# Optimization experiments

Measured on AMD Instinct MI355X. Metric: run time of the kernel, lower is better.

The kernel has to match this reference:

```python
import jax, jax.numpy as jnp
import numpy as np

N_NODES = 50000
N_EDGES = 400000
C_IN = 256
HID = 512
C_OUT = 128
N_GRAPHS = 64
BN_EPS = 1e-5


def setup_inputs() -> dict:
    key = jax.random.key(0)
    ks = jax.random.split(key, 18)
    s_in = 1.0 / np.sqrt(C_IN)
    s_h = 1.0 / np.sqrt(HID)
    inp = {
        'x': jax.random.normal(ks[0], (N_NODES, C_IN), jnp.float32),
        'edge_index': jax.random.randint(ks[1], (2, N_EDGES), 0, N_NODES, jnp.int32).astype(jnp.int64),
        'batch': jnp.sort(jax.random.randint(ks[2], (N_NODES,), 0, N_GRAPHS, jnp.int32)).astype(jnp.int64),
        'enc_w': jax.random.normal(ks[3], (C_IN, HID), jnp.float32) * s_in,
        'enc_b': jax.random.normal(ks[4], (HID,), jnp.float32) * s_in,
        'conv_w0': jax.random.normal(ks[5], (2, HID, HID), jnp.float32) * s_h,
        'conv_b0': jax.random.normal(ks[6], (2, HID), jnp.float32) * s_h,
        'bn0_g': jax.random.uniform(ks[7], (2, HID), jnp.float32, 0.5, 1.5),
        'bn0_b': jax.random.normal(ks[8], (2, HID), jnp.float32) * 0.1,
        'conv_w1': jax.random.normal(ks[9], (2, HID, HID), jnp.float32) * s_h,
        'conv_b1': jax.random.normal(ks[10], (2, HID), jnp.float32) * s_h,
        'bn1_g': jax.random.uniform(ks[11], (2, HID), jnp.float32, 0.5, 1.5),
        'bn1_b': jax.random.normal(ks[12], (2, HID), jnp.float32) * 0.1,
        'lin_w': jax.random.normal(ks[13], (HID, HID), jnp.float32) * s_h,
        'lin_b': jax.random.normal(ks[14], (HID,), jnp.float32) * s_h,
        'clf_w': jax.random.normal(ks[15], (HID, C_OUT), jnp.float32) * s_h,
        'clf_b': jax.random.normal(ks[16], (C_OUT,), jnp.float32) * s_h,
    }
    return inp


def _bn_eval(h, gamma, beta):
    # BatchNorm1d in eval mode with default buffers: running_mean=0, running_var=1
    return h * (gamma / jnp.sqrt(1.0 + BN_EPS)) + beta


def reference(x, edge_index, batch, enc_w, enc_b, conv_w0, conv_b0, bn0_g, bn0_b,
              conv_w1, conv_b1, bn1_g, bn1_b, lin_w, lin_b, clf_w, clf_b):
    src, dst = edge_index[0], edge_index[1]
    n = x.shape[0]
    # encoder (gbn output is dead code in the original forward; omitted)
    x = x @ enc_w + enc_b  # [N, HID]
    # GIN_Net: 2 GINConv layers, eps=0, sum aggregation, MLP = Lin-BN-ReLU-Lin-BN
    for i in range(2):
        agg = jax.ops.segment_sum(x[src], dst, num_segments=n)  # scatter-add of neighbor feats
        h = x + agg  # (1 + eps) * x + aggr, eps = 0
        h = h @ conv_w0[i] + conv_b0[i]
        h = jax.nn.relu(_bn_eval(h, bn0_g[i], bn0_b[i]))
        h = h @ conv_w1[i] + conv_b1[i]
        h = _bn_eval(h, bn1_g[i], bn1_b[i])
        # inter-layer relu (dropout p=0 / eval -> identity); skipped after last layer
        x = h if i == 1 else jax.nn.relu(h)
    # global mean pooling over graphs
    sums = jax.ops.segment_sum(x, batch, num_segments=N_GRAPHS)  # [G, HID]
    counts = jax.ops.segment_sum(jnp.ones((n,), x.dtype), batch, num_segments=N_GRAPHS)
    pooled = sums / jnp.maximum(counts, 1.0)[:, None]
    g = jax.nn.gelu(pooled @ lin_w + lin_b, approximate=False)
    # dropout(0.5) identity in eval mode
    return g @ clf_w + clf_b  # [G, C_OUT]
```

## Files before the change

### kernel.cpp

```cpp
#include <hip/hip_runtime.h>
#include <hip/hip_bf16.h>
#include <stdint.h>

#define NN 50000
#define M_PAD 50176
#define NE 400000
#define CIN 256
#define KF 320
#define HID 512
#define COUT 128
#define NG 64
#define SCAN_NB ((NN + 255) / 256)
#define GEMM_NWG 392

typedef short bf16x8 __attribute__((ext_vector_type(8)));
typedef float f32x4 __attribute__((ext_vector_type(4)));

__device__ inline float bf2f(unsigned short u) {
    union { unsigned int i; float f; } v; v.i = ((unsigned int)u) << 16; return v.f;
}
__device__ inline unsigned short f2bf(float f) {
    union { float f; unsigned int u; } v; v.f = f;
    unsigned int r = v.u + 0x7fffu + ((v.u >> 16) & 1u);
    return (unsigned short)(r >> 16);
}

__device__ inline void async16(const void* g, void* l) {
    __builtin_amdgcn_global_load_lds((const __attribute__((address_space(1))) void*)g,
                                     (__attribute__((address_space(3))) void*)l, 16, 0, 0);
}


__global__ void k_f32_to_bf16(const float* __restrict__ in, unsigned short* __restrict__ out, int n4) {
    int i = blockIdx.x * blockDim.x + threadIdx.x;
    if (i < n4) {
        float4 v = ((const float4*)in)[i];
        ushort4 o;
        o.x = f2bf(v.x); o.y = f2bf(v.y); o.z = f2bf(v.z); o.w = f2bf(v.w);
        ((ushort4*)out)[i] = o;
    }
}

__global__ void k_transpose_cvt(const float* __restrict__ in, unsigned short* __restrict__ out, int K, int N) {
    __shared__ float tile[32][33];
    int bx = blockIdx.x * 32, by = blockIdx.y * 32;
    int tx = threadIdx.x & 31, ty = threadIdx.x >> 5;
    for (int i = 0; i < 32; i += 8)
        tile[ty + i][tx] = in[(size_t)(by + ty + i) * N + bx + tx];
    __syncthreads();
    for (int i = 0; i < 32; i += 8)
        out[(size_t)(bx + ty + i) * K + by + tx] = f2bf(tile[tx][ty + i]);
}

__global__ void k_fuse_w0(const float* __restrict__ enc_w, const float* __restrict__ enc_b,
                          const float* __restrict__ W0, unsigned short* __restrict__ WfT) {
    int n = blockIdx.x;
    __shared__ float col[HID];
    for (int j = threadIdx.x; j < HID; j += 256) col[j] = W0[(size_t)j * HID + n];
    __syncthreads();
    int k = threadIdx.x;
    float acc = 0.f;
    for (int j = 0; j < HID; j++) acc += enc_w[(size_t)k * HID + j] * col[j];
    WfT[(size_t)n * KF + k] = f2bf(acc);
    if (k == 0) {
        float v = 0.f;
        for (int j = 0; j < HID; j++) v += enc_b[j] * col[j];
        WfT[(size_t)n * KF + 256] = f2bf(v);
    }
    if (k >= 1 && k < 64) WfT[(size_t)n * KF + 256 + k] = 0;
}

__global__ void k_affine(const float* __restrict__ enc_b,
                         const float* __restrict__ cb0, const float* __restrict__ bg0, const float* __restrict__ bb0,
                         const float* __restrict__ cb1, const float* __restrict__ bg1, const float* __restrict__ bb1,
                         float* __restrict__ scale, float* __restrict__ shift) {
    int c = threadIdx.x;
    const float inv = 0.9999950000374997f;
    scale[c] = 1.f; shift[c] = enc_b[c];
    for (int l = 0; l < 2; l++) {
        float s0 = bg0[l * HID + c] * inv;
        scale[(1 + 2 * l) * HID + c] = s0;
        shift[(1 + 2 * l) * HID + c] = cb0[l * HID + c] * s0 + bb0[l * HID + c];
        float s1 = bg1[l * HID + c] * inv;
        scale[(2 + 2 * l) * HID + c] = s1;
        shift[(2 + 2 * l) * HID + c] = cb1[l * HID + c] * s1 + bb1[l * HID + c];
    }
}


__global__ void k_hist(const int* __restrict__ dst, int* __restrict__ indeg, int n) {
    int i = blockIdx.x * blockDim.x + threadIdx.x;
    if (i < n) atomicAdd(&indeg[dst[i]], 1);
}

__global__ void k_scan1(const int* __restrict__ indeg, int* __restrict__ local,
                        int* __restrict__ blocksum, int n) {
    __shared__ int s[256];
    int t = threadIdx.x;
    int i = blockIdx.x * 256 + t;
    int v = (i < n) ? indeg[i] : 0;
    s[t] = v;
    __syncthreads();
    for (int d = 1; d < 256; d <<= 1) {
        int u = (t >= d) ? s[t - d] : 0;
        __syncthreads();
        s[t] += u;
        __syncthreads();
    }
    if (i < n) local[i] = s[t] - v;
    if (t == 255) blocksum[blockIdx.x] = s[255];
}

__global__ void k_scan2(int* __restrict__ blocksum, int nb) {
    __shared__ int s[256];
    int t = threadIdx.x;
    int v = (t < nb) ? blocksum[t] : 0;
    s[t] = v;
    __syncthreads();
    for (int d = 1; d < 256; d <<= 1) {
        int u = (t >= d) ? s[t - d] : 0;
        __syncthreads();
        s[t] += u;
        __syncthreads();
    }
    if (t < nb) blocksum[t] = s[t] - v;
}

__global__ void k_scan3(const int* __restrict__ local, const int* __restrict__ blocksum,
                        const int* __restrict__ indeg, int* __restrict__ off,
                        int* __restrict__ cursor, int n) {
    int i = blockIdx.x * 256 + threadIdx.x;
    if (i < n) {
        int o = local[i] + blocksum[blockIdx.x];
        off[i] = o;
        cursor[i] = o;
        if (i == n - 1) off[n] = o + indeg[i];
    }
}

__global__ void k_fill(const int* __restrict__ src, const int* __restrict__ dst,
                       int* __restrict__ cursor, int* __restrict__ csr, int n) {
    int i = blockIdx.x * blockDim.x + threadIdx.x;
    if (i < n) {
        int p = atomicAdd(&cursor[dst[i]], 1);
        csr[p] = src[i];
    }
}


__global__ void k_aggregate0(const unsigned short* __restrict__ x, const int* __restrict__ off,
                             const int* __restrict__ csr, unsigned short* __restrict__ z) {
    int wid = (int)((blockIdx.x * blockDim.x + threadIdx.x) >> 6);
    if (wid >= NN) return;
    int lane = threadIdx.x & 63;
    const uint2* xr = (const uint2*)x;
    uint2 v = xr[(size_t)wid * 64 + lane];
    float acc[4];
    {
        unsigned short* p = (unsigned short*)&v;
        for (int i = 0; i < 4; i++) acc[i] = bf2f(p[i]);
    }
    int e0 = off[wid], e1 = off[wid + 1];
    int e = e0;
    for (; e + 3 < e1; e += 4) {
        int u0 = csr[e], u1 = csr[e + 1], u2 = csr[e + 2], u3 = csr[e + 3];
        uint2 v0 = xr[(size_t)u0 * 64 + lane];
        uint2 v1 = xr[(size_t)u1 * 64 + lane];
        uint2 v2 = xr[(size_t)u2 * 64 + lane];
        uint2 v3 = xr[(size_t)u3 * 64 + lane];
        unsigned short* p0 = (unsigned short*)&v0;
        unsigned short* p1 = (unsigned short*)&v1;
        unsigned short* p2 = (unsigned short*)&v2;
        unsigned short* p3 = (unsigned short*)&v3;
#pragma unroll
        for (int i = 0; i < 4; i++)
            acc[i] += (bf2f(p0[i]) + bf2f(p1[i])) + (bf2f(p2[i]) + bf2f(p3[i]));
    }
    for (; e < e1; e++) {
        int u = csr[e];
        uint2 vu = xr[(size_t)u * 64 + lane];
        unsigned short* p = (unsigned short*)&vu;
#pragma unroll
        for (int i = 0; i < 4; i++) acc[i] += bf2f(p[i]);
    }
    uint2 o;
    unsigned short* po = (unsigned short*)&o;
    for (int i = 0; i < 4; i++) po[i] = f2bf(acc[i]);
    uint2* zr = (uint2*)z;
    zr[(size_t)wid * 80 + lane] = o;
    if (lane < 16) {
        uint2 ex; ex.x = 0; ex.y = 0;
        if (lane == 0) ex.x = (unsigned)f2bf((float)(1 + e1 - e0));
        zr[(size_t)wid * 80 + 64 + lane] = ex;
    }
}


__global__ void k_aggregate(const unsigned short* __restrict__ x, const int* __restrict__ off,
                            const int* __restrict__ csr, unsigned short* __restrict__ h) {
    int wid = (int)((blockIdx.x * blockDim.x + threadIdx.x) >> 6);
    if (wid >= NN) return;
    int lane = threadIdx.x & 63;
    const uint4* xr = (const uint4*)x;
    uint4 v = xr[(size_t)wid * 64 + lane];
    float acc[8];
    {
        unsigned short* p = (unsigned short*)&v;
        for (int i = 0; i < 8; i++) acc[i] = bf2f(p[i]);
    }
    int e0 = off[wid], e1 = off[wid + 1];
    int e = e0;
    for (; e + 3 < e1; e += 4) {
        int u0 = csr[e], u1 = csr[e + 1], u2 = csr[e + 2], u3 = csr[e + 3];
        uint4 v0 = xr[(size_t)u0 * 64 + lane];
        uint4 v1 = xr[(size_t)u1 * 64 + lane];
        uint4 v2 = xr[(size_t)u2 * 64 + lane];
        uint4 v3 = xr[(size_t)u3 * 64 + lane];
        unsigned short* p0 = (unsigned short*)&v0;
        unsigned short* p1 = (unsigned short*)&v1;
        unsigned short* p2 = (unsigned short*)&v2;
        unsigned short* p3 = (unsigned short*)&v3;
#pragma unroll
        for (int i = 0; i < 8; i++)
            acc[i] += (bf2f(p0[i]) + bf2f(p1[i])) + (bf2f(p2[i]) + bf2f(p3[i]));
    }
    for (; e < e1; e++) {
        int u = csr[e];
        uint4 vu = xr[(size_t)u * 64 + lane];
        unsigned short* p = (unsigned short*)&vu;
#pragma unroll
        for (int i = 0; i < 8; i++) acc[i] += bf2f(p[i]);
    }
    uint4 o;
    unsigned short* po = (unsigned short*)&o;
    for (int i = 0; i < 8; i++) po[i] = f2bf(acc[i]);
    ((uint4*)h)[(size_t)wid * 64 + lane] = o;
}


template <int RELU, int NSTEPS>
__global__ __launch_bounds__(512, 2) void k_gemm(const unsigned short* __restrict__ A,
                                                 const unsigned short* __restrict__ WT,
                                                 const float* __restrict__ scale,
                                                 const float* __restrict__ shift,
                                                 unsigned short* __restrict__ out) {
    constexpr int K = NSTEPS * 64;
    __shared__ char lds[131072];
    const int tid = threadIdx.x, w = tid >> 6, lane = tid & 63;
    const int wr = w >> 2, wc = w & 3;
    const int lr = lane & 15, lh = lane >> 4;

    int orig = blockIdx.x;
    int wgid = (orig & 7) * 49 + (orig >> 3);
    int tile_m = (wgid >> 1) * 256;
    int n0 = (wgid & 1) * 256;

    const unsigned short* gA[4];
    const unsigned short* gB[4];
    int ldsoff[4];
#pragma unroll
    for (int ci = 0; ci < 4; ci++) {
        int c = w * 4 + ci;
        int f = c >> 1, kf = c & 1;
        ldsoff[ci] = c * 1024;
        gA[ci] = A + (size_t)(tile_m + f * 16 + lr) * K + kf * 32 + lh * 8;
        gB[ci] = WT + (size_t)(n0 + f * 16 + lr) * K + kf * 32 + lh * 8;
    }

    f32x4 acc[8][4];
#pragma unroll
    for (int x = 0; x < 8; x++)
#pragma unroll
        for (int y = 0; y < 4; y++) acc[x][y] = f32x4{0.f, 0.f, 0.f, 0.f};

#pragma unroll
    for (int ci = 0; ci < 4; ci++) async16(gA[ci], lds + ldsoff[ci]);
#pragma unroll
    for (int ci = 0; ci < 4; ci++) async16(gB[ci], lds + 32768 + ldsoff[ci]);
#pragma unroll
    for (int ci = 0; ci < 4; ci++) async16(gA[ci] + 64, lds + 65536 + ldsoff[ci]);
#pragma unroll
    for (int ci = 0; ci < 4; ci++) async16(gB[ci] + 64, lds + 65536 + 32768 + ldsoff[ci]);

#pragma unroll
    for (int ks = 0; ks < NSTEPS; ks++) {
        const int cur = (ks & 1) << 16;
        if (ks < NSTEPS - 1) asm volatile("s_waitcnt vmcnt(8)" ::: "memory");
        else                 asm volatile("s_waitcnt vmcnt(0)" ::: "memory");
        __builtin_amdgcn_s_barrier();
        __builtin_amdgcn_sched_barrier(0);
#pragma unroll
        for (int kf = 0; kf < 2; kf++) {
            bf16x8 a[8], bb[4];
#pragma unroll
            for (int mf = 0; mf < 8; mf++)
                a[mf] = *(const bf16x8*)(lds + cur + ((wr * 8 + mf) * 2 + kf) * 1024 + lane * 16);
#pragma unroll
            for (int nf = 0; nf < 4; nf++)
                bb[nf] = *(const bf16x8*)(lds + cur + 32768 + ((wc * 4 + nf) * 2 + kf) * 1024 + lane * 16);
#pragma unroll
            for (int mf = 0; mf < 8; mf++)
#pragma unroll
                for (int nf = 0; nf < 4; nf++)
                    acc[mf][nf] = __builtin_amdgcn_mfma_f32_16x16x32_bf16(bb[nf], a[mf], acc[mf][nf], 0, 0, 0);
        }
        __builtin_amdgcn_sched_barrier(0);
        __builtin_amdgcn_s_barrier();
        if (ks + 2 < NSTEPS) {
            int ko = (ks + 2) << 6;
#pragma unroll
            for (int ci = 0; ci < 4; ci++) async16(gA[ci] + ko, lds + cur + ldsoff[ci]);
#pragma unroll
            for (int ci = 0; ci < 4; ci++) async16(gB[ci] + ko, lds + cur + 32768 + ldsoff[ci]);
        }
    }

#pragma unroll
    for (int nf = 0; nf < 4; nf++) {
        int col = n0 + wc * 64 + nf * 16 + lh * 4;
        float4 sc = *(const float4*)&scale[col];
        float4 sh = *(const float4*)&shift[col];
#pragma unroll
        for (int mf = 0; mf < 8; mf++) {
            int row = tile_m + wr * 128 + mf * 16 + lr;
            float y0 = acc[mf][nf][0] * sc.x + sh.x;
            float y1 = acc[mf][nf][1] * sc.y + sh.y;
            float y2 = acc[mf][nf][2] * sc.z + sh.z;
            float y3 = acc[mf][nf][3] * sc.w + sh.w;
            if (RELU) {
                y0 = fmaxf(y0, 0.f); y1 = fmaxf(y1, 0.f);
                y2 = fmaxf(y2, 0.f); y3 = fmaxf(y3, 0.f);
            }
            ushort4 pk;
            pk.x = f2bf(y0); pk.y = f2bf(y1); pk.z = f2bf(y2); pk.w = f2bf(y3);
            *(ushort4*)(out + (size_t)row * HID + col) = pk;
        }
    }
}


__global__ void k_bounds(const int* __restrict__ batch, int* __restrict__ bounds) {
    int t = threadIdx.x;
    if (t <= NG) {
        int lo = 0, hi = NN;
        while (lo < hi) { int mid = (lo + hi) >> 1; if (batch[mid] < t) lo = mid + 1; else hi = mid; }
        bounds[t] = lo;
    }
}

__global__ void k_pool(const unsigned short* __restrict__ x, const int* __restrict__ bounds,
                       float* __restrict__ pooled) {
    int g = blockIdx.x, s = blockIdx.y, t = threadIdx.x;
    int b0 = bounds[g], b1 = bounds[g + 1];
    int len = b1 - b0;
    int r0 = b0 + (int)((long long)len * s / 8);
    int r1 = b0 + (int)((long long)len * (s + 1) / 8);
    float acc = 0.f;
    for (int r = r0; r < r1; r++) acc += bf2f(x[(size_t)r * HID + t]);
    if (r1 > r0) atomicAdd(&pooled[g * HID + t], acc);
}

__global__ void k_tailgemm(const float* __restrict__ pooledSum, const int* __restrict__ bounds,
                           const float* __restrict__ W1, const float* __restrict__ scale,
                           const float* __restrict__ shift, float* __restrict__ xfp) {
    int g = blockIdx.x, t = threadIdx.x;
    __shared__ float row[HID];
    int cnt = bounds[g + 1] - bounds[g];
    float invc = 1.f / fmaxf((float)cnt, 1.f);
    row[t] = pooledSum[g * HID + t] * invc;
    __syncthreads();
    float acc = 0.f;
    for (int k = 0; k < HID; k++) acc += row[k] * W1[(size_t)k * HID + t];
    xfp[g * HID + t] = acc * scale[t] + shift[t];
}

__global__ void k_head1(const float* __restrict__ xfp, const float* __restrict__ lin_w,
                        const float* __restrict__ lin_b, float* __restrict__ gout) {
    int g = blockIdx.x, t = threadIdx.x;
    __shared__ float row[HID];
    row[t] = xfp[g * HID + t];
    __syncthreads();
    float acc = lin_b[t];
    for (int k = 0; k < HID; k++) acc += row[k] * lin_w[(size_t)k * HID + t];
    gout[g * HID + t] = 0.5f * acc * (1.f + erff(acc * 0.7071067811865475f));
}

__global__ void k_head2(const float* __restrict__ gbuf, const float* __restrict__ clf_w,
                        const float* __restrict__ clf_b, float* __restrict__ out) {
    int g = blockIdx.x, t = threadIdx.x;
    __shared__ float row[HID];
    for (int k = t; k < HID; k += 128) row[k] = gbuf[g * HID + k];
    __syncthreads();
    float acc = clf_b[t];
    for (int k = 0; k < HID; k++) acc += row[k] * clf_w[(size_t)k * COUT + t];
    out[g * COUT + t] = acc;
}


extern "C" void kernel_launch(void* const* d_in, const int* in_sizes, int n_in,
                              void* d_out, int out_size, void* d_ws, size_t ws_size,
                              hipStream_t stream) {
    const float* x_f32   = (const float*)d_in[0];
    const int*   ei      = (const int*)d_in[1];
    const int*   batch   = (const int*)d_in[2];
    const float* enc_w   = (const float*)d_in[3];
    const float* enc_b   = (const float*)d_in[4];
    const float* conv_w0 = (const float*)d_in[5];
    const float* conv_b0 = (const float*)d_in[6];
    const float* bn0_g   = (const float*)d_in[7];
    const float* bn0_b   = (const float*)d_in[8];
    const float* conv_w1 = (const float*)d_in[9];
    const float* conv_b1 = (const float*)d_in[10];
    const float* bn1_g   = (const float*)d_in[11];
    const float* bn1_b   = (const float*)d_in[12];
    const float* lin_w   = (const float*)d_in[13];
    const float* lin_b   = (const float*)d_in[14];
    const float* clf_w   = (const float*)d_in[15];
    const float* clf_b   = (const float*)d_in[16];
    const int* srcp = ei;
    const int* dstp = ei + NE;

    char* ws = (char*)d_ws;
    size_t o = 0;
    auto alloc = [&](size_t b) { size_t r = o; o += (b + 255) & ~(size_t)255; return r; };
    unsigned short* buf0 = (unsigned short*)(ws + alloc((size_t)M_PAD * HID * 2));
    unsigned short* buf1 = (unsigned short*)(ws + alloc((size_t)M_PAD * HID * 2));
    unsigned short* buf2 = (unsigned short*)(ws + alloc((size_t)M_PAD * HID * 2));
    unsigned short* xbf  = buf0;
    unsigned short* zbuf = buf2;
    unsigned short* WfT  = (unsigned short*)(ws + alloc((size_t)HID * KF * 2));
    unsigned short* c0T  = (unsigned short*)(ws + alloc((size_t)HID * HID * 2));
    unsigned short* c1T  = (unsigned short*)(ws + alloc((size_t)HID * HID * 2));
    float* aff_scale = (float*)(ws + alloc(5 * HID * 4));
    float* aff_shift = (float*)(ws + alloc(5 * HID * 4));
    int* indeg  = (int*)(ws + alloc((size_t)NN * 4));
    int* off    = (int*)(ws + alloc((size_t)(NN + 1) * 4));
    int* cursor = (int*)(ws + alloc((size_t)NN * 4));
    int* csr    = (int*)(ws + alloc((size_t)NE * 4));
    int* scan_local = (int*)(ws + alloc((size_t)NN * 4));
    int* scan_bsum  = (int*)(ws + alloc((size_t)256 * 4));
    int* bounds = (int*)(ws + alloc((size_t)(NG + 1) * 4));
    float* pooledSum = (float*)(ws + alloc((size_t)NG * HID * 4));
    float* xfp       = (float*)(ws + alloc((size_t)NG * HID * 4));
    float* gbuf      = (float*)(ws + alloc((size_t)NG * HID * 4));
    (void)ws_size; (void)n_in; (void)in_sizes; (void)out_size;

    hipMemsetAsync(indeg, 0, (size_t)NN * 4, stream);
    hipMemsetAsync(pooledSum, 0, (size_t)NG * HID * 4, stream);

    k_f32_to_bf16<<<(NN * CIN / 4 + 255) / 256, 256, 0, stream>>>(x_f32, xbf, NN * CIN / 4);
    k_fuse_w0<<<HID, 256, 0, stream>>>(enc_w, enc_b, conv_w0, WfT);
    k_transpose_cvt<<<dim3(16, 16), 256, 0, stream>>>(conv_w0 + HID * HID, c0T, HID, HID);
    k_transpose_cvt<<<dim3(16, 16), 256, 0, stream>>>(conv_w1, c1T, HID, HID);
    k_affine<<<1, 512, 0, stream>>>(enc_b, conv_b0, bn0_g, bn0_b, conv_b1, bn1_g, bn1_b,
                                    aff_scale, aff_shift);

    k_hist<<<(NE + 255) / 256, 256, 0, stream>>>(dstp, indeg, NE);
    k_scan1<<<SCAN_NB, 256, 0, stream>>>(indeg, scan_local, scan_bsum, NN);
    k_scan2<<<1, 256, 0, stream>>>(scan_bsum, SCAN_NB);
    k_scan3<<<SCAN_NB, 256, 0, stream>>>(scan_local, scan_bsum, indeg, off, cursor, NN);
    k_fill<<<(NE + 255) / 256, 256, 0, stream>>>(srcp, dstp, cursor, csr, NE);
    k_bounds<<<1, 128, 0, stream>>>(batch, bounds);

    k_aggregate0<<<(NN * 64) / 256, 256, 0, stream>>>(xbf, off, csr, zbuf);
    k_gemm<1, KF / 64><<<GEMM_NWG, 512, 0, stream>>>(zbuf, WfT,
                                                     aff_scale + 1 * HID, aff_shift + 1 * HID, buf0);
    k_gemm<1, HID / 64><<<GEMM_NWG, 512, 0, stream>>>(buf0, c1T,
                                                      aff_scale + 2 * HID, aff_shift + 2 * HID, buf2);

    k_aggregate<<<(NN * 64) / 256, 256, 0, stream>>>(buf2, off, csr, buf1);
    k_gemm<1, HID / 64><<<GEMM_NWG, 512, 0, stream>>>(buf1, c0T,
                                                      aff_scale + 3 * HID, aff_shift + 3 * HID, buf2);

    k_pool<<<dim3(NG, 8), 512, 0, stream>>>(buf2, bounds, pooledSum);
    k_tailgemm<<<NG, 512, 0, stream>>>(pooledSum, bounds, conv_w1 + HID * HID,
                                       aff_scale + 4 * HID, aff_shift + 4 * HID, xfp);
    k_head1<<<NG, 512, 0, stream>>>(xfp, lin_w, lin_b, gbuf);
    k_head2<<<NG, 128, 0, stream>>>(gbuf, clf_w, clf_b, (float*)d_out);
}
```

Before: 453.5 us.

## Merge small prep and tail kernels, fold scan pass, deepen gather unroll

Cuts the number of kernel launches. The bf16 conversion and the degree histogram become one grid, the two weight transposes share one launch, the graph-bounds search moves into the affine kernel, and the three tail matvec kernels become one. The separate block-sum scan kernel is removed: each scan3 block now reduces the preceding block sums itself. The neighbour-gather loops in both aggregation kernels unroll to 8 loads so more memory requests are in flight, at the cost of higher register pressure.

```diff
diff --git a/kernel.cpp b/kernel.cpp
--- a/kernel.cpp
+++ b/kernel.cpp
@@ -11,6 +11,8 @@
 #define COUT 128
 #define NG 64
 #define SCAN_NB ((NN + 255) / 256)
+#define CVT_NB (NN * CIN / 4 / 256)
+#define HIST_NB ((NE + 255) / 256)
 #define GEMM_NWG 392
 
 typedef short bf16x8 __attribute__((ext_vector_type(8)));
@@ -31,25 +33,33 @@
 }
 
 
-__global__ void k_f32_to_bf16(const float* __restrict__ in, unsigned short* __restrict__ out, int n4) {
-    int i = blockIdx.x * blockDim.x + threadIdx.x;
-    if (i < n4) {
-        float4 v = ((const float4*)in)[i];
+__global__ void k_prep0(const float* __restrict__ xf, unsigned short* __restrict__ xbf,
+                        const int* __restrict__ dst, int* __restrict__ indeg) {
+    int b = blockIdx.x;
+    if (b < CVT_NB) {
+        int i = b * 256 + threadIdx.x;
+        float4 v = ((const float4*)xf)[i];
         ushort4 o;
         o.x = f2bf(v.x); o.y = f2bf(v.y); o.z = f2bf(v.z); o.w = f2bf(v.w);
-        ((ushort4*)out)[i] = o;
-    }
-}
-
-__global__ void k_transpose_cvt(const float* __restrict__ in, unsigned short* __restrict__ out, int K, int N) {
+        ((ushort4*)xbf)[i] = o;
+    } else {
+        int i = (b - CVT_NB) * 256 + threadIdx.x;
+        if (i < NE) atomicAdd(&indeg[dst[i]], 1);
+    }
+}
+
+__global__ void k_transpose2(const float* __restrict__ s0, const float* __restrict__ s1,
+                             unsigned short* __restrict__ d0, unsigned short* __restrict__ d1) {
+    const float* in = blockIdx.z ? s1 : s0;
+    unsigned short* out = blockIdx.z ? d1 : d0;
     __shared__ float tile[32][33];
     int bx = blockIdx.x * 32, by = blockIdx.y * 32;
     int tx = threadIdx.x & 31, ty = threadIdx.x >> 5;
     for (int i = 0; i < 32; i += 8)
-        tile[ty + i][tx] = in[(size_t)(by + ty + i) * N + bx + tx];
+        tile[ty + i][tx] = in[(size_t)(by + ty + i) * HID + bx + tx];
     __syncthreads();
     for (int i = 0; i < 32; i += 8)
-        out[(size_t)(bx + ty + i) * K + by + tx] = f2bf(tile[tx][ty + i]);
+        out[(size_t)(bx + ty + i) * HID + by + tx] = f2bf(tile[tx][ty + i]);
 }
 
 __global__ void k_fuse_w0(const float* __restrict__ enc_w, const float* __restrict__ enc_b,
@@ -70,10 +80,11 @@
     if (k >= 1 && k < 64) WfT[(size_t)n * KF + 256 + k] = 0;
 }
 
-__global__ void k_affine(const float* __restrict__ enc_b,
-                         const float* __restrict__ cb0, const float* __restrict__ bg0, const float* __restrict__ bb0,
-                         const float* __restrict__ cb1, const float* __restrict__ bg1, const float* __restrict__ bb1,
-                         float* __restrict__ scale, float* __restrict__ shift) {
+__global__ void k_affine_bounds(const float* __restrict__ enc_b,
+                                const float* __restrict__ cb0, const float* __restrict__ bg0, const float* __restrict__ bb0,
+                                const float* __restrict__ cb1, const float* __restrict__ bg1, const float* __restrict__ bb1,
+                                float* __restrict__ scale, float* __restrict__ shift,
+                                const int* __restrict__ batch, int* __restrict__ bounds) {
     int c = threadIdx.x;
     const float inv = 0.9999950000374997f;
     scale[c] = 1.f; shift[c] = enc_b[c];
@@ -85,13 +96,13 @@
         scale[(2 + 2 * l) * HID + c] = s1;
         shift[(2 + 2 * l) * HID + c] = cb1[l * HID + c] * s1 + bb1[l * HID + c];
     }
-}
-
-
-__global__ void k_hist(const int* __restrict__ dst, int* __restrict__ indeg, int n) {
-    int i = blockIdx.x * blockDim.x + threadIdx.x;
-    if (i < n) atomicAdd(&indeg[dst[i]], 1);
-}
+    if (c <= NG) {
+        int lo = 0, hi = NN;
+        while (lo < hi) { int mid = (lo + hi) >> 1; if (batch[mid] < c) lo = mid + 1; else hi = mid; }
+        bounds[c] = lo;
+    }
+}
+
 
 __global__ void k_scan1(const int* __restrict__ indeg, int* __restrict__ local,
                         int* __restrict__ blocksum, int n) {
@@ -111,27 +122,21 @@
     if (t == 255) blocksum[blockIdx.x] = s[255];
 }
 
-__global__ void k_scan2(int* __restrict__ blocksum, int nb) {
-    __shared__ int s[256];
-    int t = threadIdx.x;
-    int v = (t < nb) ? blocksum[t] : 0;
-    s[t] = v;
-    __syncthreads();
-    for (int d = 1; d < 256; d <<= 1) {
-        int u = (t >= d) ? s[t - d] : 0;
-        __syncthreads();
-        s[t] += u;
-        __syncthreads();
-    }
-    if (t < nb) blocksum[t] = s[t] - v;
-}
-
 __global__ void k_scan3(const int* __restrict__ local, const int* __restrict__ blocksum,
                         const int* __restrict__ indeg, int* __restrict__ off,
                         int* __restrict__ cursor, int n) {
-    int i = blockIdx.x * 256 + threadIdx.x;
+    __shared__ int s[256];
+    int t = threadIdx.x;
+    s[t] = (t < blockIdx.x && t < SCAN_NB) ? blocksum[t] : 0;
+    __syncthreads();
+    for (int d = 128; d > 0; d >>= 1) {
+        if (t < d) s[t] += s[t + d];
+        __syncthreads();
+    }
+    int ps = s[0];
+    int i = blockIdx.x * 256 + t;
     if (i < n) {
-        int o = local[i] + blocksum[blockIdx.x];
+        int o = local[i] + ps;
         off[i] = o;
         cursor[i] = o;
         if (i == n - 1) off[n] = o + indeg[i];
@@ -162,19 +167,16 @@
     }
     int e0 = off[wid], e1 = off[wid + 1];
     int e = e0;
-    for (; e + 3 < e1; e += 4) {
-        int u0 = csr[e], u1 = csr[e + 1], u2 = csr[e + 2], u3 = csr[e + 3];
-        uint2 v0 = xr[(size_t)u0 * 64 + lane];
-        uint2 v1 = xr[(size_t)u1 * 64 + lane];
-        uint2 v2 = xr[(size_t)u2 * 64 + lane];
-        uint2 v3 = xr[(size_t)u3 * 64 + lane];
-        unsigned short* p0 = (unsigned short*)&v0;
-        unsigned short* p1 = (unsigned short*)&v1;
-        unsigned short* p2 = (unsigned short*)&v2;
-        unsigned short* p3 = (unsigned short*)&v3;
-#pragma unroll
-        for (int i = 0; i < 4; i++)
-            acc[i] += (bf2f(p0[i]) + bf2f(p1[i])) + (bf2f(p2[i]) + bf2f(p3[i]));
+    for (; e + 7 < e1; e += 8) {
+        uint2 vv[8];
+#pragma unroll
+        for (int q = 0; q < 8; q++) vv[q] = xr[(size_t)csr[e + q] * 64 + lane];
+#pragma unroll
+        for (int q = 0; q < 8; q++) {
+            unsigned short* p = (unsigned short*)&vv[q];
+#pragma unroll
+            for (int i = 0; i < 4; i++) acc[i] += bf2f(p[i]);
+        }
     }
     for (; e < e1; e++) {
         int u = csr[e];
@@ -210,19 +212,16 @@
     }
     int e0 = off[wid], e1 = off[wid + 1];
     int e = e0;
-    for (; e + 3 < e1; e += 4) {
-        int u0 = csr[e], u1 = csr[e + 1], u2 = csr[e + 2], u3 = csr[e + 3];
-        uint4 v0 = xr[(size_t)u0 * 64 + lane];
-        uint4 v1 = xr[(size_t)u1 * 64 + lane];
-        uint4 v2 = xr[(size_t)u2 * 64 + lane];
-        uint4 v3 = xr[(size_t)u3 * 64 + lane];
-        unsigned short* p0 = (unsigned short*)&v0;
-        unsigned short* p1 = (unsigned short*)&v1;
-        unsigned short* p2 = (unsigned short*)&v2;
-        unsigned short* p3 = (unsigned short*)&v3;
-#pragma unroll
-        for (int i = 0; i < 8; i++)
-            acc[i] += (bf2f(p0[i]) + bf2f(p1[i])) + (bf2f(p2[i]) + bf2f(p3[i]));
+    for (; e + 7 < e1; e += 8) {
+        uint4 vv[8];
+#pragma unroll
+        for (int q = 0; q < 8; q++) vv[q] = xr[(size_t)csr[e + q] * 64 + lane];
+#pragma unroll
+        for (int q = 0; q < 8; q++) {
+            unsigned short* p = (unsigned short*)&vv[q];
+#pragma unroll
+            for (int i = 0; i < 8; i++) acc[i] += bf2f(p[i]);
+        }
     }
     for (; e < e1; e++) {
         int u = csr[e];
@@ -339,15 +338,6 @@
 }
 
 
-__global__ void k_bounds(const int* __restrict__ batch, int* __restrict__ bounds) {
-    int t = threadIdx.x;
-    if (t <= NG) {
-        int lo = 0, hi = NN;
-        while (lo < hi) { int mid = (lo + hi) >> 1; if (batch[mid] < t) lo = mid + 1; else hi = mid; }
-        bounds[t] = lo;
-    }
-}
-
 __global__ void k_pool(const unsigned short* __restrict__ x, const int* __restrict__ bounds,
                        float* __restrict__ pooled) {
     int g = blockIdx.x, s = blockIdx.y, t = threadIdx.x;
@@ -360,40 +350,35 @@
     if (r1 > r0) atomicAdd(&pooled[g * HID + t], acc);
 }
 
-__global__ void k_tailgemm(const float* __restrict__ pooledSum, const int* __restrict__ bounds,
-                           const float* __restrict__ W1, const float* __restrict__ scale,
-                           const float* __restrict__ shift, float* __restrict__ xfp) {
+__global__ void k_tail(const float* __restrict__ pooledSum, const int* __restrict__ bounds,
+                       const float* __restrict__ W1, const float* __restrict__ scale,
+                       const float* __restrict__ shift,
+                       const float* __restrict__ lin_w, const float* __restrict__ lin_b,
+                       const float* __restrict__ clf_w, const float* __restrict__ clf_b,
+                       float* __restrict__ out) {
     int g = blockIdx.x, t = threadIdx.x;
-    __shared__ float row[HID];
+    __shared__ float r0[HID], r1[HID], r2[HID];
     int cnt = bounds[g + 1] - bounds[g];
     float invc = 1.f / fmaxf((float)cnt, 1.f);
-    row[t] = pooledSum[g * HID + t] * invc;
-    __syncthreads();
-    float acc = 0.f;
-    for (int k = 0; k < HID; k++) acc += row[k] * W1[(size_t)k * HID + t];
-    xfp[g * HID + t] = acc * scale[t] + shift[t];
-}
-
-__global__ void k_head1(const float* __restrict__ xfp, const float* __restrict__ lin_w,
-                        const float* __restrict__ lin_b, float* __restrict__ gout) {
-    int g = blockIdx.x, t = threadIdx.x;
-    __shared__ float row[HID];
-    row[t] = xfp[g * HID + t];
-    __syncthreads();
-    float acc = lin_b[t];
-    for (int k = 0; k < HID; k++) acc += row[k] * lin_w[(size_t)k * HID + t];
-    gout[g * HID + t] = 0.5f * acc * (1.f + erff(acc * 0.7071067811865475f));
-}
-
-__global__ void k_head2(const float* __restrict__ gbuf, const float* __restrict__ clf_w,
-                        const float* __restrict__ clf_b, float* __restrict__ out) {
-    int g = blockIdx.x, t = threadIdx.x;
-    __shared__ float row[HID];
-    for (int k = t; k < HID; k += 128) row[k] = gbuf[g * HID + k];
-    __syncthreads();
-    float acc = clf_b[t];
-    for (int k = 0; k < HID; k++) acc += row[k] * clf_w[(size_t)k * COUT + t];
-    out[g * COUT + t] = acc;
+    r0[t] = pooledSum[g * HID + t] * invc;
+    __syncthreads();
+    {
+        float acc = 0.f;
+        for (int k = 0; k < HID; k++) acc += r0[k] * W1[(size_t)k * HID + t];
+        r1[t] = acc * scale[t] + shift[t];
+    }
+    __syncthreads();
+    {
+        float acc = lin_b[t];
+        for (int k = 0; k < HID; k++) acc += r1[k] * lin_w[(size_t)k * HID + t];
+        r2[t] = 0.5f * acc * (1.f + erff(acc * 0.7071067811865475f));
+    }
+    __syncthreads();
+    if (t < COUT) {
+        float acc = clf_b[t];
+        for (int k = 0; k < HID; k++) acc += r2[k] * clf_w[(size_t)k * COUT + t];
+        out[g * COUT + t] = acc;
+    }
 }
 
 
@@ -441,26 +426,20 @@
     int* scan_bsum  = (int*)(ws + alloc((size_t)256 * 4));
     int* bounds = (int*)(ws + alloc((size_t)(NG + 1) * 4));
     float* pooledSum = (float*)(ws + alloc((size_t)NG * HID * 4));
-    float* xfp       = (float*)(ws + alloc((size_t)NG * HID * 4));
-    float* gbuf      = (float*)(ws + alloc((size_t)NG * HID * 4));
     (void)ws_size; (void)n_in; (void)in_sizes; (void)out_size;
 
     hipMemsetAsync(indeg, 0, (size_t)NN * 4, stream);
     hipMemsetAsync(pooledSum, 0, (size_t)NG * HID * 4, stream);
 
-    k_f32_to_bf16<<<(NN * CIN / 4 + 255) / 256, 256, 0, stream>>>(x_f32, xbf, NN * CIN / 4);
+    k_prep0<<<CVT_NB + HIST_NB, 256, 0, stream>>>(x_f32, xbf, dstp, indeg);
     k_fuse_w0<<<HID, 256, 0, stream>>>(enc_w, enc_b, conv_w0, WfT);
-    k_transpose_cvt<<<dim3(16, 16), 256, 0, stream>>>(conv_w0 + HID * HID, c0T, HID, HID);
-    k_transpose_cvt<<<dim3(16, 16), 256, 0, stream>>>(conv_w1, c1T, HID, HID);
-    k_affine<<<1, 512, 0, stream>>>(enc_b, conv_b0, bn0_g, bn0_b, conv_b1, bn1_g, bn1_b,
-                                    aff_scale, aff_shift);
-
-    k_hist<<<(NE + 255) / 256, 256, 0, stream>>>(dstp, indeg, NE);
+    k_transpose2<<<dim3(16, 16, 2), 256, 0, stream>>>(conv_w0 + HID * HID, conv_w1, c0T, c1T);
+    k_affine_bounds<<<1, 512, 0, stream>>>(enc_b, conv_b0, bn0_g, bn0_b, conv_b1, bn1_g, bn1_b,
+                                           aff_scale, aff_shift, batch, bounds);
+
     k_scan1<<<SCAN_NB, 256, 0, stream>>>(indeg, scan_local, scan_bsum, NN);
-    k_scan2<<<1, 256, 0, stream>>>(scan_bsum, SCAN_NB);
     k_scan3<<<SCAN_NB, 256, 0, stream>>>(scan_local, scan_bsum, indeg, off, cursor, NN);
-    k_fill<<<(NE + 255) / 256, 256, 0, stream>>>(srcp, dstp, cursor, csr, NE);
-    k_bounds<<<1, 128, 0, stream>>>(batch, bounds);
+    k_fill<<<HIST_NB, 256, 0, stream>>>(srcp, dstp, cursor, csr, NE);
 
     k_aggregate0<<<(NN * 64) / 256, 256, 0, stream>>>(xbf, off, csr, zbuf);
     k_gemm<1, KF / 64><<<GEMM_NWG, 512, 0, stream>>>(zbuf, WfT,
@@ -473,8 +452,7 @@
                                                       aff_scale + 3 * HID, aff_shift + 3 * HID, buf2);
 
     k_pool<<<dim3(NG, 8), 512, 0, stream>>>(buf2, bounds, pooledSum);
-    k_tailgemm<<<NG, 512, 0, stream>>>(pooledSum, bounds, conv_w1 + HID * HID,
-                                       aff_scale + 4 * HID, aff_shift + 4 * HID, xfp);
-    k_head1<<<NG, 512, 0, stream>>>(xfp, lin_w, lin_b, gbuf);
-    k_head2<<<NG, 128, 0, stream>>>(gbuf, clf_w, clf_b, (float*)d_out);
-}
+    k_tail<<<NG, 512, 0, stream>>>(pooledSum, bounds, conv_w1 + HID * HID,
+                                   aff_scale + 4 * HID, aff_shift + 4 * HID,
+                                   lin_w, lin_b, clf_w, clf_b, (float*)d_out);
+}
```

After: 445.2 us. No clear change (-1.8%).
